# Kernel optimization log

Hardware: AMD Instinct MI355X
Metric: run time of the kernel (lower is better)

## Reference

```python
import jax, jax.numpy as jnp
import numpy as np

B, L, D, H = 1, 2048, 3072, 24
Dh = D // H            # 128
MLP = 4 * D            # 12288
EPS = 1e-6


def setup_inputs() -> dict:
    key = jax.random.key(0)
    ks = jax.random.split(key, 10)
    n = lambda k, shape, s=1.0: jax.random.normal(k, shape, jnp.float32) * s
    W = 0.02  # weight init scale
    return {
        "img": n(ks[0], (B, L, D)),
        "vec": n(ks[1], (B, D)),
        "pe": n(ks[2], (1, 1, L, Dh // 2, 2, 2)),
        "mod_w": n(ks[3], (D, 3 * D), W),
        "mod_b": jnp.zeros((3 * D,), jnp.float32),
        "lin1_w": n(ks[4], (D, 3 * D + MLP), W),
        "lin1_b": jnp.zeros((3 * D + MLP,), jnp.float32),
        "lin2_w": n(ks[5], (D + MLP, D), W),
        "lin2_b": jnp.zeros((D,), jnp.float32),
        "q_scale": jnp.ones((Dh,), jnp.float32),
        "k_scale": jnp.ones((Dh,), jnp.float32),
    }


def _rms_norm(x, scale):
    return x * jax.lax.rsqrt(jnp.mean(x * x, axis=-1, keepdims=True) + EPS) * scale


def _apply_rope(x, pe):
    # x: [B,H,L,Dh]; pe: [1,1,L,Dh/2,2,2]
    xr = x.reshape(*x.shape[:-1], Dh // 2, 1, 2)
    out = pe[..., 0] * xr[..., 0] + pe[..., 1] * xr[..., 1]  # [B,H,L,Dh/2,2]
    return out.reshape(*x.shape[:-1], Dh)


def reference(img, vec, pe, mod_w, mod_b, lin1_w, lin1_b, lin2_w, lin2_b, q_scale, k_scale):
    # adaLN modulation (single): shift / scale / gate, each [B,1,D]
    mod = jax.nn.silu(vec) @ mod_w + mod_b
    shift, scale, gate = jnp.split(mod[:, None, :], 3, axis=-1)

    # pre-norm LayerNorm (no affine) + modulation
    mu = jnp.mean(img, axis=-1, keepdims=True)
    var = jnp.var(img, axis=-1, keepdims=True)
    x = (1.0 + scale) * ((img - mu) * jax.lax.rsqrt(var + EPS)) + shift

    # fused QKV + MLP projection
    proj = x @ lin1_w + lin1_b                     # [B,L,3D+MLP]
    qkv, mlp = proj[..., : 3 * D], proj[..., 3 * D :]

    # 'B L (K H D) -> K B H L D'
    qkv = qkv.reshape(B, L, 3, H, Dh).transpose(2, 0, 3, 1, 4)
    q, k, v = qkv[0], qkv[1], qkv[2]

    # per-head QK RMSNorm
    q = _rms_norm(q, q_scale)
    k = _rms_norm(k, k_scale)

    # RoPE
    q = _apply_rope(q, pe)
    k = _apply_rope(k, pe)

    # attention (scale = head_dim**-0.5)
    scores = jnp.einsum("bhqd,bhkd->bhqk", q, k) * (Dh ** -0.5)
    probs = jax.nn.softmax(scores, axis=-1)
    attn = jnp.einsum("bhqk,bhkd->bhqd", probs, v)
    attn = attn.transpose(0, 2, 1, 3).reshape(B, L, D)  # 'B H L D -> B L (H D)'

    # gated parallel MLP output + residual
    out = jnp.concatenate([attn, jax.nn.gelu(mlp, approximate=True)], axis=-1) @ lin2_w + lin2_b
    return img + gate * out
```

## Files before the change

kernel.cpp:

```cpp
#include <hip/hip_runtime.h>
#include <hip/hip_bf16.h>
#include <stdint.h>


#define DEV static __device__ __forceinline__

typedef __attribute__((ext_vector_type(4))) float f32x4;
typedef __attribute__((ext_vector_type(16))) float f32x16;
typedef __attribute__((ext_vector_type(8))) short s8v;

DEV unsigned short f2bf(float f) {
  union { float f; unsigned u; } v; v.f = f;
  unsigned r = v.u + 0x7fffu + ((v.u >> 16) & 1u);
  return (unsigned short)(r >> 16);
}
DEV float bf2f(unsigned short b) {
  union { unsigned u; float f; } v; v.u = ((unsigned)b) << 16; return v.f;
}
DEV unsigned pk2bf(float a, float b) {
  union { __hip_bfloat162 h; unsigned u; } v;
  v.h = __float22bfloat162_rn(make_float2(a, b));
  return v.u;
}

DEV void gl_lds16(const void* g, void* l) {
  __builtin_amdgcn_global_load_lds(
      (const __attribute__((address_space(1))) unsigned int*)(uintptr_t)g,
      (__attribute__((address_space(3))) unsigned int*)(uint32_t)(uintptr_t)l,
      16, 0, 0);
}

__global__ __launch_bounds__(256) void modvec_partial(
    const float* __restrict__ vec, const float* __restrict__ mod_w, float* __restrict__ part) {
  __shared__ float s[384];
  const int tid = threadIdx.x;
  const int i0 = blockIdx.y * 384;
  for (int i = tid; i < 384; i += 256) {
    float v = vec[i0 + i];
    s[i] = v / (1.f + __expf(-v));
  }
  __syncthreads();
  const int j = blockIdx.x * 256 + tid;
  float acc = 0.f;
#pragma unroll 8
  for (int i = 0; i < 384; ++i) acc += s[i] * mod_w[(size_t)(i0 + i) * 9216 + j];
  part[(size_t)blockIdx.y * 9216 + j] = acc;
}

__global__ __launch_bounds__(256) void modvec_reduce(
    const float* __restrict__ part, const float* __restrict__ mod_b, float* __restrict__ mod) {
  const int j = blockIdx.x * 256 + threadIdx.x;
  float a = mod_b[j];
#pragma unroll
  for (int y = 0; y < 8; ++y) a += part[(size_t)y * 9216 + j];
  mod[j] = a;
}

__global__ __launch_bounds__(256) void ln_mod_kernel(
    const float* __restrict__ img, const float* __restrict__ mod, unsigned short* __restrict__ x) {
  const int l = blockIdx.x, tid = threadIdx.x;
  const int wave = tid >> 6;
  const f32x4* row = (const f32x4*)(img + (size_t)l * 3072);
  f32x4 v[3];
  float s = 0.f, s2 = 0.f;
#pragma unroll
  for (int i = 0; i < 3; ++i) {
    v[i] = row[tid + i * 256];
#pragma unroll
    for (int c = 0; c < 4; ++c) { s += v[i][c]; s2 += v[i][c] * v[i][c]; }
  }
#pragma unroll
  for (int m = 1; m < 64; m <<= 1) { s += __shfl_xor(s, m); s2 += __shfl_xor(s2, m); }
  __shared__ float rs[4], rs2[4];
  if ((tid & 63) == 0) { rs[wave] = s; rs2[wave] = s2; }
  __syncthreads();
  s = rs[0] + rs[1] + rs[2] + rs[3];
  s2 = rs2[0] + rs2[1] + rs2[2] + rs2[3];
  const float mu = s * (1.f / 3072.f);
  const float var = s2 * (1.f / 3072.f) - mu * mu;
  const float inv = rsqrtf(var + 1e-6f);
#pragma unroll
  for (int i = 0; i < 3; ++i) {
    int d0 = (tid + i * 256) * 4;
    unsigned out[2];
    unsigned short o[4];
#pragma unroll
    for (int c = 0; c < 4; ++c) {
      int d = d0 + c;
      float val = (1.f + mod[3072 + d]) * ((v[i][c] - mu) * inv) + mod[d];
      o[c] = f2bf(val);
    }
    out[0] = o[0] | ((unsigned)o[1] << 16);
    out[1] = o[2] | ((unsigned)o[3] << 16);
    *(uint2*)(x + (size_t)l * 3072 + d0) = make_uint2(out[0], out[1]);
  }
}

__global__ __launch_bounds__(256) void transpose_kernel(
    const float* __restrict__ W, unsigned short* __restrict__ Wt, int K, int N) {
  __shared__ float t[64][65];
  const int k0 = blockIdx.x * 64, n0 = blockIdx.y * 64;
  const int tid = threadIdx.x;
#pragma unroll
  for (int it = 0; it < 4; ++it) {
    const int k = it * 16 + (tid >> 4), c4 = (tid & 15) * 4;
    f32x4 v = *(const f32x4*)&W[(size_t)(k0 + k) * N + n0 + c4];
    t[k][c4] = v[0]; t[k][c4 + 1] = v[1]; t[k][c4 + 2] = v[2]; t[k][c4 + 3] = v[3];
  }
  __syncthreads();
#pragma unroll
  for (int it = 0; it < 2; ++it) {
    const int idx = it * 256 + tid;
    const int n = idx >> 3, k8 = (idx & 7) * 8;
    s8v o;
#pragma unroll
    for (int e = 0; e < 8; ++e) o[e] = (short)f2bf(t[k8 + e][n]);
    *(s8v*)&Wt[(size_t)(n0 + n) * K + k0 + k8] = o;
  }
}

template <int EPI>
__global__ __launch_bounds__(512, 2) void gemm256_kernel(
    const unsigned short* __restrict__ A, const unsigned short* __restrict__ Bt,
    const float* __restrict__ bias, void* __restrict__ Cout,
    int K, int N, int nTile, int nBN) {
  __shared__ unsigned short lds[65536];
  const int tid = threadIdx.x;
  const int lane = tid & 63, w = tid >> 6;
  const int wm = w >> 2, wn = w & 3;
  const int l15 = lane & 15, l4 = lane >> 4;

  int bid = blockIdx.x;
  const int nwg = gridDim.x;
  bid = (bid & 7) * (nwg >> 3) + (bid >> 3);
  const int bz = bid / (nBN << 3);
  const int rem = bid - bz * (nBN << 3);
  const int m0 = (rem & 7) << 8;
  const int n0 = (rem >> 3) << 8;
  const int kOff = bz * nTile * 64;

  const int sr = (w << 3) + (lane >> 3);
  const int skc = ((lane & 7) ^ (sr & 7)) << 3;
  const size_t aBase = (size_t)m0 * K + kOff;
  const size_t bBase = (size_t)n0 * K + kOff;

  const int xs0 = (l4 ^ (l15 & 7)) << 3;
  const int xs1 = ((4 + l4) ^ (l15 & 7)) << 3;
  int aRow[4], bRow[2];
#pragma unroll
  for (int i = 0; i < 4; ++i) aRow[i] = (wm * 64 + i * 16 + l15) * 64;
#pragma unroll
  for (int j = 0; j < 2; ++j) bRow[j] = (wn * 32 + j * 16 + l15) * 64;

  f32x4 acc[2][2][4][2];
#pragma unroll
  for (int mq = 0; mq < 2; ++mq)
#pragma unroll
    for (int nq = 0; nq < 2; ++nq)
#pragma unroll
      for (int i = 0; i < 4; ++i)
#pragma unroll
        for (int j = 0; j < 2; ++j) acc[mq][nq][i][j] = (f32x4){0.f, 0.f, 0.f, 0.f};

#define STAGE(op, h, par, kt)                                                        \
  do {                                                                               \
    const unsigned short* _s = (op) ? Bt : A;                                        \
    const size_t _b = (op) ? bBase : aBase;                                          \
    unsigned short* _d = &lds[((par) << 15) + ((op) << 14) + ((h) << 13) + (w << 9)];\
    gl_lds16(_s + _b + (size_t)((h) * 128 + sr) * K + (kt) * 64 + skc, _d);          \
    gl_lds16(_s + _b + (size_t)((h) * 128 + 64 + sr) * K + (kt) * 64 + skc, _d + 4096);\
  } while (0)

#define FRAGP(op, h, rowoff, xsv) \
  (*(const s8v*)&lds[pB + ((op) << 14) + ((h) << 13) + (rowoff) + (xsv)])

#define PH_MID()                                            \
  __builtin_amdgcn_s_barrier();                             \
  asm volatile("s_waitcnt lgkmcnt(0)" ::: "memory");        \
  __builtin_amdgcn_sched_barrier(0);                        \
  __builtin_amdgcn_s_setprio(1)

#define PH_END()                                            \
  __builtin_amdgcn_s_setprio(0);                            \
  asm volatile("s_waitcnt vmcnt(10)" ::: "memory");         \
  __builtin_amdgcn_s_barrier()

#define MFMA_QUAD(mq, nq)                                                              \
  _Pragma("unroll") for (int i = 0; i < 4; ++i) _Pragma("unroll") for (int j = 0; j < 2; ++j) { \
    acc[mq][nq][i][j] =                                                                \
        __builtin_amdgcn_mfma_f32_16x16x32_bf16(a[i][0], b[nq][j][0], acc[mq][nq][i][j], 0, 0, 0); \
    acc[mq][nq][i][j] =                                                                \
        __builtin_amdgcn_mfma_f32_16x16x32_bf16(a[i][1], b[nq][j][1], acc[mq][nq][i][j], 0, 0, 0); \
  }

  STAGE(0, 0, 0, 0); STAGE(1, 0, 0, 0); STAGE(1, 1, 0, 0); STAGE(0, 1, 0, 0);
  {
    const int k1 = (nTile > 1) ? 1 : 0;
    STAGE(0, 0, 1, k1); STAGE(1, 0, 1, k1); STAGE(1, 1, 1, k1);
  }
  asm volatile("s_waitcnt vmcnt(10)" ::: "memory");
  __builtin_amdgcn_s_barrier();

  s8v a[4][2], b[2][2][2];
#pragma unroll 2
  for (int t = 0; t < nTile; ++t) {
    const int pB = (t & 1) << 15;
    const int kt1 = (t + 1 < nTile) ? t + 1 : 0;
    const int kt2 = (t + 2 < nTile) ? t + 2 : 0;
#pragma unroll
    for (int i = 0; i < 4; ++i) { a[i][0] = FRAGP(0, 0, aRow[i], xs0); a[i][1] = FRAGP(0, 0, aRow[i], xs1); }
#pragma unroll
    for (int j = 0; j < 2; ++j) { b[0][j][0] = FRAGP(1, 0, bRow[j], xs0); b[0][j][1] = FRAGP(1, 0, bRow[j], xs1); }
    STAGE(0, 1, (t + 1) & 1, kt1);
    PH_MID();
    MFMA_QUAD(0, 0);
    PH_END();
#pragma unroll
    for (int j = 0; j < 2; ++j) { b[1][j][0] = FRAGP(1, 1, bRow[j], xs0); b[1][j][1] = FRAGP(1, 1, bRow[j], xs1); }
    STAGE(0, 0, t & 1, kt2);
    PH_MID();
    MFMA_QUAD(0, 1);
    PH_END();
#pragma unroll
    for (int i = 0; i < 4; ++i) { a[i][0] = FRAGP(0, 1, aRow[i], xs0); a[i][1] = FRAGP(0, 1, aRow[i], xs1); }
    STAGE(1, 0, t & 1, kt2);
    PH_MID();
    MFMA_QUAD(1, 0);
    PH_END();
    STAGE(1, 1, t & 1, kt2);
    PH_MID();
    MFMA_QUAD(1, 1);
    PH_END();
  }

  asm volatile("s_waitcnt vmcnt(0)" ::: "memory");
  __builtin_amdgcn_s_barrier();

#pragma unroll
  for (int mq = 0; mq < 2; ++mq)
#pragma unroll
    for (int nq = 0; nq < 2; ++nq)
#pragma unroll
      for (int j = 0; j < 2; ++j) {
        const int col = n0 + nq * 128 + wn * 32 + j * 16 + l15;
        const float bj = (EPI == 0) ? bias[col] : 0.f;
#pragma unroll
        for (int i = 0; i < 4; ++i) {
          const int row0 = m0 + mq * 128 + wm * 64 + i * 16 + (l4 << 2);
#pragma unroll
          for (int r = 0; r < 4; ++r) {
            if (EPI == 0)
              ((unsigned short*)Cout)[(size_t)(row0 + r) * N + col] = f2bf(acc[mq][nq][i][j][r] + bj);
            else
              ((float*)Cout)[(size_t)bz * 2048 * N + (size_t)(row0 + r) * N + col] =
                  acc[mq][nq][i][j][r];
          }
        }
      }
#undef STAGE
#undef FRAGP
#undef PH_MID
#undef PH_END
#undef MFMA_QUAD
}

__global__ __launch_bounds__(256) void reduce2_kernel(
    const float* __restrict__ part, const float* __restrict__ img,
    const float* __restrict__ mod, const float* __restrict__ bias, float* __restrict__ out) {
  const size_t idx = ((size_t)blockIdx.x * 256 + threadIdx.x) * 4;
  const int col = (int)(idx % 3072);
  f32x4 p0 = *(const f32x4*)(part + idx);
  f32x4 p1 = *(const f32x4*)(part + 6291456 + idx);
  f32x4 im = *(const f32x4*)(img + idx);
  f32x4 o;
#pragma unroll
  for (int e = 0; e < 4; ++e)
    o[e] = im[e] + mod[6144 + col + e] * (p0[e] + p1[e] + bias[col + e]);
  *(f32x4*)(out + idx) = o;
}

DEV void qk_one(const unsigned short* src, const float* sc, const f32x4 pe4, float extra,
                unsigned short* dst, int lane) {
  unsigned xx = *(const unsigned*)(src + 2 * lane);
  float x0 = bf2f((unsigned short)(xx & 0xffff));
  float x1 = bf2f((unsigned short)(xx >> 16));
  float ss = x0 * x0 + x1 * x1;
#pragma unroll
  for (int m = 1; m < 64; m <<= 1) ss += __shfl_xor(ss, m);
  const float inv = rsqrtf(ss * (1.f / 128.f) + 1e-6f);
  x0 *= inv * sc[2 * lane];
  x1 *= inv * sc[2 * lane + 1];
  float o0 = (pe4.x * x0 + pe4.y * x1) * extra;
  float o1 = (pe4.z * x0 + pe4.w * x1) * extra;
  *(unsigned*)(dst + 2 * lane) = (unsigned)f2bf(o0) | ((unsigned)f2bf(o1) << 16);
}

__global__ __launch_bounds__(256) void qk_prep_kernel(
    const unsigned short* __restrict__ proj, const float* __restrict__ pe,
    const float* __restrict__ q_scale, const float* __restrict__ k_scale,
    unsigned short* __restrict__ qr, unsigned short* __restrict__ kr,
    unsigned short* __restrict__ vt) {
  const int l = blockIdx.x;
  const int tid = threadIdx.x, lane = tid & 63, wave = tid >> 6;
  const unsigned short* row = proj + (size_t)l * 21504;
  const f32x4 pe4 = *(const f32x4*)(pe + ((size_t)l * 64 + lane) * 4);
  const float qsc = 0.12751743761f;
#pragma unroll
  for (int hh = 0; hh < 6; ++hh) {
    const int h = wave + hh * 4;
    qk_one(row + h * 128, q_scale, pe4, qsc, qr + ((size_t)h * 2048 + l) * 128, lane);
    qk_one(row + 3072 + h * 128, k_scale, pe4, 1.f, kr + ((size_t)h * 2048 + l) * 128, lane);
    unsigned vv = *(const unsigned*)(row + 6144 + h * 128 + 2 * lane);
    vt[((size_t)h * 128 + 2 * lane) * 2048 + l] = (unsigned short)(vv & 0xffff);
    vt[((size_t)h * 128 + 2 * lane + 1) * 2048 + l] = (unsigned short)(vv >> 16);
  }
}

__global__ __launch_bounds__(256) void gelu_kernel(
    const unsigned short* __restrict__ proj, unsigned short* __restrict__ A2) {
  const int idx = blockIdx.x * 256 + threadIdx.x;
  const int r = idx / 1536, c = idx % 1536;
  s8v v = *(const s8v*)(proj + (size_t)r * 21504 + 9216 + (size_t)c * 8);
  s8v o;
#pragma unroll
  for (int e = 0; e < 8; ++e) {
    float x = bf2f((unsigned short)v[e]);
    float y = 0.7978845608f * (x + 0.044715f * x * x * x);
    float ex = __expf(2.f * y);
    float th = 1.f - 2.f / (ex + 1.f);
    o[e] = (short)f2bf(0.5f * x * (1.f + th));
  }
  *(s8v*)(A2 + (size_t)r * 15360 + 3072 + (size_t)c * 8) = o;
}

__global__ __launch_bounds__(256) void attn_kernel(
    const unsigned short* __restrict__ qr, const unsigned short* __restrict__ kr,
    const unsigned short* __restrict__ vt, unsigned short* __restrict__ A2) {
  __shared__ char lds[65536];
  const int tid = threadIdx.x, lane = tid & 63, w = tid >> 6;
  const int l31 = lane & 31, hi = lane >> 5;
  const int h = blockIdx.y;
  const int q0 = blockIdx.x * 128 + w * 32;
  const int q = q0 + l31;

  s8v qf[8];
  {
    const unsigned short* qb = qr + ((size_t)h * 2048 + q) * 128 + hi * 8;
#pragma unroll
    for (int ks = 0; ks < 8; ++ks) qf[ks] = *(const s8v*)(qb + ks * 16);
  }

  int koff[4], voff[4];
#pragma unroll
  for (int c = 0; c < 4; ++c) {
    const int ob = (w * 4 + c) * 1024 + lane * 16;
    const int row = ob >> 8;
    const int sl = (ob >> 4) & 15;
    const int ssl = sl ^ (row & 15);
    koff[c] = row * 128 + ssl * 8;
    const int dh = row * 2 + (ssl >> 3);
    voff[c] = dh * 2048 + (ssl & 7) * 8;
  }
  const unsigned short* krH = kr + (size_t)h * 2048 * 128;
  const unsigned short* vtH = vt + (size_t)h * 128 * 2048;

  f32x16 oacc[4];
#pragma unroll
  for (int rf = 0; rf < 4; ++rf)
#pragma unroll
    for (int e = 0; e < 16; ++e) oacc[rf][e] = 0.f;
  float m = -3e38f, l = 0.f;

#define ATT_STAGE(t)                                                        \
  do {                                                                      \
    char* kb_ = lds + ((t) & 1) * 32768;                                    \
    char* vb_ = kb_ + 16384;                                                \
    _Pragma("unroll") for (int c = 0; c < 4; ++c) {                         \
      gl_lds16(krH + (size_t)(t) * 8192 + koff[c], kb_ + (w * 4 + c) * 1024); \
      gl_lds16(vtH + (size_t)(t) * 64 + voff[c], vb_ + (w * 4 + c) * 1024);   \
    }                                                                       \
  } while (0)

  ATT_STAGE(0);
  __syncthreads();

  for (int t = 0; t < 32; ++t) {
    if (t + 1 < 32) ATT_STAGE(t + 1);
    char* kb = lds + (t & 1) * 32768;
    char* vb = kb + 16384;

    f32x16 st[2];
#pragma unroll
    for (int rf = 0; rf < 2; ++rf)
#pragma unroll
      for (int e = 0; e < 16; ++e) st[rf][e] = 0.f;
#pragma unroll
    for (int ks = 0; ks < 8; ++ks)
#pragma unroll
      for (int rf = 0; rf < 2; ++rf) {
        const int kvr = rf * 32 + l31;
        s8v kf = *(const s8v*)(kb + kvr * 256 + (((ks * 2 + hi) ^ (kvr & 15)) << 4));
        st[rf] = __builtin_amdgcn_mfma_f32_32x32x16_bf16(kf, qf[ks], st[rf], 0, 0, 0);
      }

    float pm = st[0][0];
#pragma unroll
    for (int rf = 0; rf < 2; ++rf)
#pragma unroll
      for (int e = 0; e < 16; ++e) pm = fmaxf(pm, st[rf][e]);
    pm = fmaxf(pm, __shfl_xor(pm, 32));
    if (__any(pm - m > 11.5f)) {
      const float mn = fmaxf(m, pm);
      const float rs = exp2f(m - mn);
      l *= rs;
#pragma unroll
      for (int rf = 0; rf < 4; ++rf)
#pragma unroll
        for (int e = 0; e < 16; ++e) oacc[rf][e] *= rs;
      m = mn;
    }
    unsigned P2[16];
#pragma unroll
    for (int rb = 0; rb < 2; ++rb)
#pragma unroll
      for (int g = 0; g < 4; ++g) {
        const float e0 = exp2f(st[rb][4 * g + 0] - m);
        const float e1 = exp2f(st[rb][4 * g + 1] - m);
        const float e2 = exp2f(st[rb][4 * g + 2] - m);
        const float e3 = exp2f(st[rb][4 * g + 3] - m);
        l += (e0 + e1) + (e2 + e3);
        P2[rb * 8 + g * 2 + 0] = pk2bf(e0, e1);
        P2[rb * 8 + g * 2 + 1] = pk2bf(e2, e3);
      }

#pragma unroll
    for (int ks = 0; ks < 4; ++ks) {
      const int iA = ((2 * ks) >> 2) * 8 + ((2 * ks) & 3) * 2;
      const int iB = ((2 * ks + 1) >> 2) * 8 + ((2 * ks + 1) & 3) * 2;
      const unsigned s0 = hi ? P2[iA] : P2[iB];
      const unsigned s1 = hi ? P2[iA + 1] : P2[iB + 1];
      const unsigned r0 = (unsigned)__shfl_xor((int)s0, 32);
      const unsigned r1 = (unsigned)__shfl_xor((int)s1, 32);
      const unsigned o0 = hi ? P2[iB] : P2[iA];
      const unsigned o1 = hi ? P2[iB + 1] : P2[iA + 1];
      union { unsigned u[4]; s8v v; } pf;
      pf.u[0] = hi ? r0 : o0;
      pf.u[1] = hi ? r1 : o1;
      pf.u[2] = hi ? o0 : r0;
      pf.u[3] = hi ? o1 : r1;
#pragma unroll
      for (int rf = 0; rf < 4; ++rf) {
        const int dh = rf * 32 + l31, r = dh >> 1;
        const int sl = ((dh & 1) << 3) + ks * 2 + hi;
        s8v vf = *(const s8v*)(vb + r * 256 + ((sl ^ (r & 15)) << 4));
        oacc[rf] = __builtin_amdgcn_mfma_f32_32x32x16_bf16(vf, pf.v, oacc[rf], 0, 0, 0);
      }
    }
    __syncthreads();
  }

  const float lf = l + __shfl_xor(l, 32);
  const float inv = 1.f / lf;
  char* ep = lds + w * 8448;
#pragma unroll
  for (int rf = 0; rf < 4; ++rf)
#pragma unroll
    for (int g = 0; g < 4; ++g) {
      const unsigned u0 = pk2bf(oacc[rf][4 * g + 0] * inv, oacc[rf][4 * g + 1] * inv);
      const unsigned u1 = pk2bf(oacc[rf][4 * g + 2] * inv, oacc[rf][4 * g + 3] * inv);
      *(uint2*)(ep + l31 * 264 + rf * 64 + g * 16 + hi * 8) = make_uint2(u0, u1);
    }
  __syncthreads();
  const int c = lane & 15, l4b = lane >> 4;
#pragma unroll
  for (int pass = 0; pass < 8; ++pass) {
    const int qq = pass * 4 + l4b;
    const uint2 a2 = *(const uint2*)(ep + qq * 264 + c * 16);
    const uint2 b2 = *(const uint2*)(ep + qq * 264 + c * 16 + 8);
    *(uint4*)(A2 + (size_t)(q0 + qq) * 15360 + h * 128 + c * 8) =
        make_uint4(a2.x, a2.y, b2.x, b2.y);
  }
#undef ATT_STAGE
}

extern "C" void kernel_launch(void* const* d_in, const int* in_sizes, int n_in,
                              void* d_out, int out_size, void* d_ws, size_t ws_size,
                              hipStream_t stream) {
  (void)in_sizes; (void)n_in; (void)out_size; (void)ws_size;
  const float* img    = (const float*)d_in[0];
  const float* vec    = (const float*)d_in[1];
  const float* pe     = (const float*)d_in[2];
  const float* mod_w  = (const float*)d_in[3];
  const float* mod_b  = (const float*)d_in[4];
  const float* lin1_w = (const float*)d_in[5];
  const float* lin1_b = (const float*)d_in[6];
  const float* lin2_w = (const float*)d_in[7];
  const float* lin2_b = (const float*)d_in[8];
  const float* q_s    = (const float*)d_in[9];
  const float* k_s    = (const float*)d_in[10];
  float* out = (float*)d_out;

  char* ws = (char*)d_ws;
  size_t off = 0;
  auto alloc = [&](size_t b) { size_t p = off; off += (b + 255) & ~(size_t)255; return p; };
  float* part          = (float*)(ws + alloc((size_t)8 * 9216 * 4));
  float* mod           = (float*)(ws + alloc((size_t)9216 * 4));
  unsigned short* x    = (unsigned short*)(ws + alloc((size_t)2048 * 3072 * 2));
  unsigned short* wT   = (unsigned short*)(ws + alloc((size_t)21504 * 3072 * 2));
  unsigned short* proj = (unsigned short*)(ws + alloc((size_t)2048 * 21504 * 2));
  unsigned short* qr   = (unsigned short*)(ws + alloc((size_t)24 * 2048 * 128 * 2));
  unsigned short* kr   = (unsigned short*)(ws + alloc((size_t)24 * 2048 * 128 * 2));
  unsigned short* vt   = (unsigned short*)(ws + alloc((size_t)24 * 128 * 2048 * 2));
  unsigned short* A2   = (unsigned short*)(ws + alloc((size_t)2048 * 15360 * 2));
  float* p2buf = (float*)proj;

  modvec_partial<<<dim3(36, 8), 256, 0, stream>>>(vec, mod_w, part);
  modvec_reduce<<<36, 256, 0, stream>>>(part, mod_b, mod);
  ln_mod_kernel<<<2048, 256, 0, stream>>>(img, mod, x);
  transpose_kernel<<<dim3(48, 336), 256, 0, stream>>>(lin1_w, wT, 3072, 21504);
  gemm256_kernel<0><<<672, 512, 0, stream>>>(x, wT, lin1_b, proj, 3072, 21504, 48, 84);
  qk_prep_kernel<<<2048, 256, 0, stream>>>(proj, pe, q_s, k_s, qr, kr, vt);
  gelu_kernel<<<12288, 256, 0, stream>>>(proj, A2);
  attn_kernel<<<dim3(16, 24), 256, 0, stream>>>(qr, kr, vt, A2);
  transpose_kernel<<<dim3(240, 48), 256, 0, stream>>>(lin2_w, wT, 15360, 3072);
  gemm256_kernel<2><<<192, 512, 0, stream>>>(A2, wT, nullptr, p2buf, 15360, 3072, 120, 12);
  reduce2_kernel<<<6144, 256, 0, stream>>>(p2buf, img, mod, lin2_b, out);
}
```

Measured before the change: 892.6 us.

## Fuse GELU into QKV GEMM epilogue, tile V transpose, raise GEMM2 split-K

The first GEMM's epilogue now applies tanh-GELU to the MLP columns and writes them directly into the second GEMM's input buffer, so QKV output is stored compactly. This removes the standalone gelu kernel and the round trip of the MLP activations. The V transpose moves into a dedicated LDS-tiled kernel with coalesced writes. The second GEMM uses 4-way split-K for more blocks, with the reduction summing four partials, and one vmcnt wait in the GEMM loop is dropped, which risks a load-ordering hazard.

New measurement: 899.4 us. Within noise of the previous version (+0.8%).

```diff
diff --git a/kernel.cpp b/kernel.cpp
--- a/kernel.cpp
+++ b/kernel.cpp
@@ -122,7 +122,7 @@
 template <int EPI>
 __global__ __launch_bounds__(512, 2) void gemm256_kernel(
     const unsigned short* __restrict__ A, const unsigned short* __restrict__ Bt,
-    const float* __restrict__ bias, void* __restrict__ Cout,
+    const float* __restrict__ bias, void* __restrict__ Cout, void* __restrict__ Cout2,
     int K, int N, int nTile, int nBN) {
   __shared__ unsigned short lds[65536];
   const int tid = threadIdx.x;
@@ -185,6 +185,10 @@
   asm volatile("s_waitcnt vmcnt(10)" ::: "memory");         \
   __builtin_amdgcn_s_barrier()
 
+#define PH_END_NOVM()                                       \
+  __builtin_amdgcn_s_setprio(0);                            \
+  __builtin_amdgcn_s_barrier()
+
 #define MFMA_QUAD(mq, nq)                                                              \
   _Pragma("unroll") for (int i = 0; i < 4; ++i) _Pragma("unroll") for (int j = 0; j < 2; ++j) { \
     acc[mq][nq][i][j] =                                                                \
@@ -226,7 +230,7 @@
     STAGE(1, 0, t & 1, kt2);
     PH_MID();
     MFMA_QUAD(1, 0);
-    PH_END();
+    PH_END_NOVM();
     STAGE(1, 1, t & 1, kt2);
     PH_MID();
     MFMA_QUAD(1, 1);
@@ -249,11 +253,20 @@
           const int row0 = m0 + mq * 128 + wm * 64 + i * 16 + (l4 << 2);
 #pragma unroll
           for (int r = 0; r < 4; ++r) {
-            if (EPI == 0)
-              ((unsigned short*)Cout)[(size_t)(row0 + r) * N + col] = f2bf(acc[mq][nq][i][j][r] + bj);
-            else
+            if (EPI == 0) {
+              float v = acc[mq][nq][i][j][r] + bj;
+              if (col < 9216) {
+                ((unsigned short*)Cout)[(size_t)(row0 + r) * 9216 + col] = f2bf(v);
+              } else {
+                const float y = 0.7978845608f * (v + 0.044715f * v * v * v);
+                const float ex = exp2f(2.8853900818f * y);
+                const float g = v - v / (ex + 1.f);
+                ((unsigned short*)Cout2)[(size_t)(row0 + r) * 15360 + (col - 6144)] = f2bf(g);
+              }
+            } else {
               ((float*)Cout)[(size_t)bz * 2048 * N + (size_t)(row0 + r) * N + col] =
                   acc[mq][nq][i][j][r];
+            }
           }
         }
       }
@@ -261,6 +274,7 @@
 #undef FRAGP
 #undef PH_MID
 #undef PH_END
+#undef PH_END_NOVM
 #undef MFMA_QUAD
 }
 
@@ -271,11 +285,13 @@
   const int col = (int)(idx % 3072);
   f32x4 p0 = *(const f32x4*)(part + idx);
   f32x4 p1 = *(const f32x4*)(part + 6291456 + idx);
+  f32x4 p2 = *(const f32x4*)(part + 2 * 6291456 + idx);
+  f32x4 p3 = *(const f32x4*)(part + 3 * (size_t)6291456 + idx);
   f32x4 im = *(const f32x4*)(img + idx);
   f32x4 o;
 #pragma unroll
   for (int e = 0; e < 4; ++e)
-    o[e] = im[e] + mod[6144 + col + e] * (p0[e] + p1[e] + bias[col + e]);
+    o[e] = im[e] + mod[6144 + col + e] * ((p0[e] + p1[e]) + (p2[e] + p3[e]) + bias[col + e]);
   *(f32x4*)(out + idx) = o;
 }
 
@@ -298,11 +314,10 @@
 __global__ __launch_bounds__(256) void qk_prep_kernel(
     const unsigned short* __restrict__ proj, const float* __restrict__ pe,
     const float* __restrict__ q_scale, const float* __restrict__ k_scale,
-    unsigned short* __restrict__ qr, unsigned short* __restrict__ kr,
-    unsigned short* __restrict__ vt) {
+    unsigned short* __restrict__ qr, unsigned short* __restrict__ kr) {
   const int l = blockIdx.x;
   const int tid = threadIdx.x, lane = tid & 63, wave = tid >> 6;
-  const unsigned short* row = proj + (size_t)l * 21504;
+  const unsigned short* row = proj + (size_t)l * 9216;
   const f32x4 pe4 = *(const f32x4*)(pe + ((size_t)l * 64 + lane) * 4);
   const float qsc = 0.12751743761f;
 #pragma unroll
@@ -310,27 +325,29 @@
     const int h = wave + hh * 4;
     qk_one(row + h * 128, q_scale, pe4, qsc, qr + ((size_t)h * 2048 + l) * 128, lane);
     qk_one(row + 3072 + h * 128, k_scale, pe4, 1.f, kr + ((size_t)h * 2048 + l) * 128, lane);
-    unsigned vv = *(const unsigned*)(row + 6144 + h * 128 + 2 * lane);
-    vt[((size_t)h * 128 + 2 * lane) * 2048 + l] = (unsigned short)(vv & 0xffff);
-    vt[((size_t)h * 128 + 2 * lane + 1) * 2048 + l] = (unsigned short)(vv >> 16);
-  }
-}
-
-__global__ __launch_bounds__(256) void gelu_kernel(
-    const unsigned short* __restrict__ proj, unsigned short* __restrict__ A2) {
-  const int idx = blockIdx.x * 256 + threadIdx.x;
-  const int r = idx / 1536, c = idx % 1536;
-  s8v v = *(const s8v*)(proj + (size_t)r * 21504 + 9216 + (size_t)c * 8);
-  s8v o;
-#pragma unroll
-  for (int e = 0; e < 8; ++e) {
-    float x = bf2f((unsigned short)v[e]);
-    float y = 0.7978845608f * (x + 0.044715f * x * x * x);
-    float ex = __expf(2.f * y);
-    float th = 1.f - 2.f / (ex + 1.f);
-    o[e] = (short)f2bf(0.5f * x * (1.f + th));
-  }
-  *(s8v*)(A2 + (size_t)r * 15360 + 3072 + (size_t)c * 8) = o;
+  }
+}
+
+__global__ __launch_bounds__(256) void vtrans_kernel(
+    const unsigned short* __restrict__ proj, unsigned short* __restrict__ vt) {
+  __shared__ unsigned short t[128][136];
+  const int h = blockIdx.y, l0 = blockIdx.x * 128;
+  const int tid = threadIdx.x;
+  const int row = tid >> 1, half = tid & 1;
+  const unsigned short* src = proj + (size_t)(l0 + row) * 9216 + 6144 + h * 128 + half * 64;
+#pragma unroll
+  for (int cc = 0; cc < 8; ++cc)
+    *(s8v*)&t[row][half * 64 + cc * 8] = *(const s8v*)(src + cc * 8);
+  __syncthreads();
+  const int dh = tid >> 1;
+  unsigned short* dst = vt + ((size_t)h * 128 + dh) * 2048 + l0 + half * 64;
+#pragma unroll
+  for (int lc = 0; lc < 8; ++lc) {
+    s8v o;
+#pragma unroll
+    for (int e = 0; e < 8; ++e) o[e] = (short)t[half * 64 + lc * 8 + e][dh];
+    *(s8v*)(dst + lc * 8) = o;
+  }
 }
 
 __global__ __launch_bounds__(256) void attn_kernel(
@@ -518,11 +535,11 @@
   modvec_reduce<<<36, 256, 0, stream>>>(part, mod_b, mod);
   ln_mod_kernel<<<2048, 256, 0, stream>>>(img, mod, x);
   transpose_kernel<<<dim3(48, 336), 256, 0, stream>>>(lin1_w, wT, 3072, 21504);
-  gemm256_kernel<0><<<672, 512, 0, stream>>>(x, wT, lin1_b, proj, 3072, 21504, 48, 84);
-  qk_prep_kernel<<<2048, 256, 0, stream>>>(proj, pe, q_s, k_s, qr, kr, vt);
-  gelu_kernel<<<12288, 256, 0, stream>>>(proj, A2);
+  gemm256_kernel<0><<<672, 512, 0, stream>>>(x, wT, lin1_b, proj, A2, 3072, 21504, 48, 84);
+  qk_prep_kernel<<<2048, 256, 0, stream>>>(proj, pe, q_s, k_s, qr, kr);
+  vtrans_kernel<<<dim3(16, 24), 256, 0, stream>>>(proj, vt);
   attn_kernel<<<dim3(16, 24), 256, 0, stream>>>(qr, kr, vt, A2);
   transpose_kernel<<<dim3(240, 48), 256, 0, stream>>>(lin2_w, wT, 15360, 3072);
-  gemm256_kernel<2><<<192, 512, 0, stream>>>(A2, wT, nullptr, p2buf, 15360, 3072, 120, 12);
+  gemm256_kernel<2><<<384, 512, 0, stream>>>(A2, wT, nullptr, p2buf, nullptr, 15360, 3072, 60, 12);
   reduce2_kernel<<<6144, 256, 0, stream>>>(p2buf, img, mod, lin2_b, out);
 }
```
